# Performance work log

Hardware: AMD Instinct MI355X
Metric: run time of the kernel (lower is better)

Reference implementation:

```python
import jax, jax.numpy as jnp
import numpy as np
from jax import lax

B, S, H, SS, DS = 512, 200, 128, 2, 2  # batch, seq_len, hidden, static_size, dynamic_size

def _xavier(k, shape):
    fan_in, fan_out = shape[-1], shape[0]
    lim = float(np.sqrt(6.0 / (fan_in + fan_out)))
    return jax.random.uniform(k, shape, jnp.float32, -lim, lim)

def setup_inputs() -> dict:
    key = jax.random.key(0)
    ks = jax.random.split(key, 20)
    return {
        "static":  jax.random.uniform(ks[0], (B, SS, S), jnp.float32),
        "dynamic": jax.random.uniform(ks[1], (B, DS, S), jnp.float32),
        # Encoder: 1x1 Conv1d weights stored as [H, C] (kernel dim squeezed)
        "sW": _xavier(ks[2], (H, SS)),  "sb": jnp.zeros((H,), jnp.float32),
        "dW": _xavier(ks[3], (H, DS)),  "db": jnp.zeros((H,), jnp.float32),
        # Decoder learned initial output / hidden
        "x0": _xavier(ks[4], (1, SS)),  "h0": _xavier(ks[5], (1, H)),
        # Decoder input embedding Linear(SS -> H)
        "Wemb": _xavier(ks[6], (H, SS)), "bemb": jnp.zeros((H,), jnp.float32),
        # GRU (1 layer): torch layout [3H, H] gates ordered (r, z, n)
        "Wih": _xavier(ks[7], (3 * H, H)), "Whh": _xavier(ks[8], (3 * H, H)),
        "bih": jnp.zeros((3 * H,), jnp.float32), "bhh": jnp.zeros((3 * H,), jnp.float32),
        # Attention: v [H], W [H, 3H]
        "Wa": _xavier(ks[9], (H, 3 * H)), "va": _xavier(ks[10], (1, H))[0],
        # Decoder pointer head: v [H], W [H, 2H]
        "Wd": _xavier(ks[11], (H, 2 * H)), "vd": _xavier(ks[12], (1, H))[0],
    }

def _decode(static, dynamic, sW, sb, dW, db, x0, h0, Wemb, bemb,
            Wih, Whh, bih, bhh, Wa, va, Wd, vd):
    # Encoder: 1x1 convs == per-node linear maps  -> [B, H, S]
    static_enc  = jnp.einsum('hc,bcs->bhs', sW, static)  + sb[None, :, None]
    dynamic_enc = jnp.einsum('hc,bcs->bhs', dW, dynamic) + db[None, :, None]

    keys = jax.random.split(jax.random.key(42), S)  # one sample key per decode step
    static_sg = lax.stop_gradient(static)           # mirrors static.data gather in torch

    def step(carry, key):
        last_out, h = carry                              # [B,SS], [B,H]
        emb = last_out @ Wemb.T + bemb                   # [B,H]
        # GRU cell (torch gate order r, z, n)
        gi = emb @ Wih.T + bih                           # [B,3H]
        gh = h @ Whh.T + bhh
        r = jax.nn.sigmoid(gi[:, :H] + gh[:, :H])
        z = jax.nn.sigmoid(gi[:, H:2 * H] + gh[:, H:2 * H])
        n = jnp.tanh(gi[:, 2 * H:] + r * gh[:, 2 * H:])
        h_new = (1.0 - z) * n + z * h                    # [B,H]
        # Additive attention over nodes (vectorized over batch)
        hid = jnp.broadcast_to(h_new[:, :, None], (B, H, S))
        energy = jnp.concatenate([static_enc, dynamic_enc, hid], axis=1)   # [B,3H,S]
        attn = jax.nn.softmax(
            jnp.einsum('h,bhs->bs', va, jnp.tanh(jnp.einsum('hk,bks->bhs', Wa, energy))),
            axis=1)                                      # [B,S]
        context = jnp.einsum('bs,bhs->bh', attn, static_enc)               # [B,H]
        ctx = jnp.concatenate(
            [static_enc, jnp.broadcast_to(context[:, :, None], (B, H, S))], axis=1)  # [B,2H,S]
        logits = jnp.einsum('h,bhs->bs', vd,
                            jnp.tanh(jnp.einsum('hk,bks->bhs', Wd, ctx)))  # [B,S]
        # mask is all ones (mask_fn=None) -> log(mask)=0
        probs = jax.nn.softmax(logits, axis=1)
        idx = jax.random.categorical(key, logits, axis=1)                  # [B] int
        next_out = jnp.take_along_axis(static_sg, idx[:, None, None], axis=2)[:, :, 0]  # [B,SS]
        chosen_p = jnp.take_along_axis(probs, idx[:, None], axis=1)[:, 0]  # [B]
        return (next_out, h_new), (idx, chosen_p)

    init = (jnp.broadcast_to(x0, (B, SS)), jnp.broadcast_to(h0, (B, H)))
    _, (idx_seq, prob_seq) = lax.scan(step, init, keys)
    return idx_seq.T, prob_seq.T                          # [B,S] each

def reference(static, dynamic, sW, sb, dW, db, x0, h0, Wemb, bemb,
              Wih, Whh, bih, bhh, Wa, va, Wd, vd):
    return _decode(static, dynamic, sW, sb, dW, db, x0, h0, Wemb, bemb,
                   Wih, Whh, bih, bhh, Wa, va, Wd, vd)
```

## Files before the change

kernel.cpp:

```cpp
#include <hip/hip_runtime.h>
#include <stdint.h>
#include <math.h>

#define NB 512
#define NS 200
#define NH 128
#define NH3 384
#define NWAVE 8

#define IDX4(h) ((h) + (((h) >> 6) << 2))
#define IDX1(h) ((h) + (((h) >> 6) << 4))

__device__ __forceinline__ float xla_tanhf(float x) {
  float cx = fminf(fmaxf(x, -9.0f), 9.0f);
  float x2 = __fmul_rn(cx, cx);
  float p = -2.76076847742355e-16f;
  p = __fadd_rn(__fmul_rn(x2, p), 2.00018790482477e-13f);
  p = __fadd_rn(__fmul_rn(x2, p), -8.60467152213735e-11f);
  p = __fadd_rn(__fmul_rn(x2, p), 5.12229709037114e-08f);
  p = __fadd_rn(__fmul_rn(x2, p), 1.48572235717979e-05f);
  p = __fadd_rn(__fmul_rn(x2, p), 6.37261928875436e-04f);
  p = __fadd_rn(__fmul_rn(x2, p), 4.89352455891786e-03f);
  p = __fmul_rn(cx, p);
  float q = 1.19825839466702e-06f;
  q = __fadd_rn(__fmul_rn(x2, q), 1.18534705686654e-04f);
  q = __fadd_rn(__fmul_rn(x2, q), 2.26843463243900e-03f);
  q = __fadd_rn(__fmul_rn(x2, q), 4.89352518554385e-03f);
  float r = __fdiv_rn(p, q);
  return (fabsf(x) < 0.0004f) ? x : r;
}

__device__ __forceinline__ float xla_sigmoidf(float x) {
  return __fadd_rn(0.5f, __fmul_rn(0.5f, xla_tanhf(__fmul_rn(0.5f, x))));
}

__device__ __forceinline__ float fast_tanhf(float x) {
  float e = __expf(__fmul_rn(x, 2.0f));
  float r = __builtin_amdgcn_rcpf(__fadd_rn(e, 1.0f));
  return fmaf(-2.0f, r, 1.0f);
}

__device__ __forceinline__ uint32_t rotl32(uint32_t v, int r) {
  return (v << r) | (v >> (32 - r));
}
__device__ __forceinline__ void threefry2x32(uint32_t k0, uint32_t k1,
                                             uint32_t x0, uint32_t x1,
                                             uint32_t& o0, uint32_t& o1) {
  uint32_t k2 = k0 ^ k1 ^ 0x1BD11BDAu;
  x0 += k0; x1 += k1;
  #define TFR(r) { x0 += x1; x1 = rotl32(x1, r); x1 ^= x0; }
  TFR(13) TFR(15) TFR(26) TFR(6)
  x0 += k1; x1 += k2 + 1u;
  TFR(17) TFR(29) TFR(16) TFR(24)
  x0 += k2; x1 += k0 + 2u;
  TFR(13) TFR(15) TFR(26) TFR(6)
  x0 += k0; x1 += k1 + 3u;
  TFR(17) TFR(29) TFR(16) TFR(24)
  x0 += k1; x1 += k2 + 4u;
  TFR(13) TFR(15) TFR(26) TFR(6)
  x0 += k2; x1 += k0 + 5u;
  #undef TFR
  o0 = x0; o1 = x1;
}

__device__ __forceinline__ float bits_to_gumbel(uint32_t bits) {
  const float kTiny = 1.1754943508222875e-38f;
  float f = __fsub_rn(__uint_as_float((bits >> 9) | 0x3F800000u), 1.0f);
  float u = __fadd_rn(__fmul_rn(f, __fsub_rn(1.0f, kTiny)), kTiny);
  u = fmaxf(kTiny, u);
  return -logf(-logf(u));
}

__global__ __launch_bounds__(512, 4) void k_decode(
    const float* __restrict__ stat, const float* __restrict__ dyn,
    const float* __restrict__ sW,   const float* __restrict__ sb,
    const float* __restrict__ dW,   const float* __restrict__ db,
    const float* __restrict__ x0,   const float* __restrict__ h0,
    const float* __restrict__ Wemb, const float* __restrict__ bemb,
    const float* __restrict__ Wih,  const float* __restrict__ Whh,
    const float* __restrict__ bih,  const float* __restrict__ bhh,
    const float* __restrict__ Wa,   const float* __restrict__ va,
    const float* __restrict__ Wd,   const float* __restrict__ vd,
    float* __restrict__ out) {

  __shared__ __align__(16) float st0L[NS], st1L[NS], dy0L[NS], dy1L[NS];
  __shared__ float4 AF4p[132];
  __shared__ float4 DF4p[132];
  __shared__ float4 CW4[NH];
  __shared__ float  vaP[144];
  __shared__ float  AcL[NH];
  __shared__ float WembL[2*NH], bembL[NH];
  __shared__ float bihL[NH3], bhhL[NH3];
  __shared__ __align__(16) float embL[NH], hL[NH];
  __shared__ float giL[NH3], ghL[NH3];
  __shared__ float HtLp[144];
  __shared__ float ex2L[NS];
  __shared__ uint32_t keysL[2*NS];
  __shared__ float xpL[2];
  __shared__ float part[NWAVE][8];
  __shared__ int   partI[NWAVE];

  const int t = threadIdx.x;
  const int b = blockIdx.x;
  const int w = t >> 6;
  const int s = t >> 1;
  const int h0i = (t & 1) * 64;
  const int b4 = h0i + ((h0i >> 6) << 2);
  const int b1 = h0i + ((h0i >> 6) << 4);
  const bool activeS = (t < 2*NS);

  if (t < NS) {
    st0L[t] = stat[(size_t)b*2*NS + t];
    st1L[t] = stat[(size_t)b*2*NS + NS + t];
    dy0L[t] = dyn[(size_t)b*2*NS + t];
    dy1L[t] = dyn[(size_t)b*2*NS + NS + t];
    uint32_t q0, q1;
    threefry2x32(0u, 42u, 0u, (uint32_t)t, q0, q1);
    keysL[2*t] = q0; keysL[2*t + 1] = q1;
  }
  if (t < NH) {
    int h = t;
    const float* war = Wa + (size_t)h * NH3;
    float as0 = 0.f, as1 = 0.f, ad0 = 0.f, ad1 = 0.f, ac = 0.f;
    for (int k = 0; k < NH; ++k) {
      as0 = fmaf(war[k],     sW[k*2+0], as0);
      as1 = fmaf(war[k],     sW[k*2+1], as1);
      ad0 = fmaf(war[NH+k],  dW[k*2+0], ad0);
      ad1 = fmaf(war[NH+k],  dW[k*2+1], ad1);
      ac  = fmaf(war[k],     sb[k],     ac);
    }
    for (int k = 0; k < NH; ++k) ac = fmaf(war[NH+k], db[k], ac);
    AF4p[IDX4(h)] = make_float4(as0, as1, ad0, ad1);
    vaP[IDX1(h)] = va[h];
    AcL[h] = ac;

    const float* wdr = Wd + (size_t)h * 256;
    float ds0 = 0.f, ds1 = 0.f, dc = 0.f, c0 = 0.f, c1 = 0.f, cb = 0.f;
    for (int k = 0; k < NH; ++k) {
      ds0 = fmaf(wdr[k],    sW[k*2+0], ds0);
      ds1 = fmaf(wdr[k],    sW[k*2+1], ds1);
      dc  = fmaf(wdr[k],    sb[k],     dc);
      c0  = fmaf(wdr[NH+k], sW[k*2+0], c0);
      c1  = fmaf(wdr[NH+k], sW[k*2+1], c1);
      cb  = fmaf(wdr[NH+k], sb[k],     cb);
    }
    DF4p[IDX4(h)] = make_float4(ds0, ds1, vd[h], dc);
    CW4[h] = make_float4(c0, c1, cb, 0.f);

    bembL[h] = bemb[h];
    WembL[2*h]   = Wemb[2*h];
    WembL[2*h+1] = Wemb[2*h+1];
    hL[h] = h0[h];
  }
  for (int i = t; i < NH3; i += 512) { bihL[i] = bih[i]; bhhL[i] = bhh[i]; }
  if (t == 0) { xpL[0] = x0[0]; xpL[1] = x0[1]; }
  __syncthreads();

  float s0r = 0.f, s1r = 0.f, d0r = 0.f, d1r = 0.f;
  if (activeS) { s0r = st0L[s]; s1r = st1L[s]; d0r = dy0L[s]; d1r = dy1L[s]; }

  for (int step = 0; step < NS; ++step) {
    if (t < NH) {
      float e = fmaf(xpL[1], WembL[t*2+1], __fmul_rn(xpL[0], WembL[t*2+0]));
      embL[t] = __fadd_rn(e, bembL[t]);
    }
    __syncthreads();

    if (t < 256) {
      const float4* wp0 = (const float4*)(Wih + (size_t)t * NH);
      const float4* wp1 = (const float4*)(Whh + (size_t)(NH + t) * NH);
      const float4* e4 = (const float4*)embL;
      const float4* h4 = (const float4*)hL;
      float a0 = 0.f, a1 = 0.f;
      #pragma unroll 8
      for (int k4 = 0; k4 < 32; ++k4) {
        float4 c0 = wp0[k4], c1 = wp1[k4];
        float4 ev = e4[k4],  hv = h4[k4];
        a0 = fmaf(c0.x, ev.x, a0); a0 = fmaf(c0.y, ev.y, a0);
        a0 = fmaf(c0.z, ev.z, a0); a0 = fmaf(c0.w, ev.w, a0);
        a1 = fmaf(c1.x, hv.x, a1); a1 = fmaf(c1.y, hv.y, a1);
        a1 = fmaf(c1.z, hv.z, a1); a1 = fmaf(c1.w, hv.w, a1);
      }
      giL[t]      = __fadd_rn(a0, bihL[t]);
      ghL[NH + t] = __fadd_rn(a1, bhhL[NH + t]);
    } else {
      const bool isWih = (t < NH3);
      const float4* wp = isWih
          ? (const float4*)(Wih + (size_t)t * NH)
          : (const float4*)(Whh + (size_t)(t - NH3) * NH);
      const float4* op = isWih ? (const float4*)embL : (const float4*)hL;
      float a0 = 0.f;
      #pragma unroll 8
      for (int k4 = 0; k4 < 32; ++k4) {
        float4 c = wp[k4], v = op[k4];
        a0 = fmaf(c.x, v.x, a0); a0 = fmaf(c.y, v.y, a0);
        a0 = fmaf(c.z, v.z, a0); a0 = fmaf(c.w, v.w, a0);
      }
      if (isWih) giL[t]       = __fadd_rn(a0, bihL[t]);
      else       ghL[t - NH3] = __fadd_rn(a0, bhhL[t - NH3]);
    }
    __syncthreads();

    if (t < NH) {
      float r = xla_sigmoidf(__fadd_rn(giL[t],      ghL[t]));
      float z = xla_sigmoidf(__fadd_rn(giL[t+NH],   ghL[t+NH]));
      float n = xla_tanhf(__fadd_rn(giL[t+2*NH], __fmul_rn(r, ghL[t+2*NH])));
      float hv = hL[t];
      hL[t] = __fadd_rn(__fmul_rn(__fsub_rn(1.0f, z), n), __fmul_rn(z, hv));
    }
    __syncthreads();

    if (t < NH) {
      const float4* war = (const float4*)(Wa + (size_t)t*NH3 + 2*NH);
      const float4* hn4 = (const float4*)hL;
      float acc = 0.f;
      #pragma unroll 8
      for (int k4 = 0; k4 < 32; ++k4) {
        float4 a = war[k4], hv = hn4[k4];
        acc = fmaf(a.x, hv.x, acc); acc = fmaf(a.y, hv.y, acc);
        acc = fmaf(a.z, hv.z, acc); acc = fmaf(a.w, hv.w, acc);
      }
      HtLp[IDX1(t)] = __fadd_rn(acc, AcL[t]);
    }
    __syncthreads();

    float acc = 0.f;
    if (activeS) {
      #pragma unroll 4
      for (int j = 0; j < 64; ++j) {
        float4 af = AF4p[b4 + j];
        float vah = vaP[b1 + j];
        float ath = HtLp[b1 + j];
        float e = fmaf(af.y, s1r, __fmul_rn(af.x, s0r));
        e = fmaf(af.z, d0r, e);
        e = fmaf(af.w, d1r, e);
        e = __fadd_rn(e, ath);
        acc = fmaf(vah, fast_tanhf(e), acc);
      }
    }
    float sc = activeS ? __fadd_rn(acc, __shfl_xor(acc, 1)) : 0.f;

    float exv = activeS ? __expf(sc) : 0.f;
    {
      float sm = exv;
      float c0 = __fmul_rn(exv, s0r);
      float c1 = __fmul_rn(exv, s1r);
      #pragma unroll
      for (int mm = 2; mm < 64; mm <<= 1) {
        sm = __fadd_rn(sm, __shfl_xor(sm, mm));
        c0 = __fadd_rn(c0, __shfl_xor(c0, mm));
        c1 = __fadd_rn(c1, __shfl_xor(c1, mm));
      }
      if ((t & 63) == 0) { part[w][0] = sm; part[w][1] = c0; part[w][2] = c1; }
    }
    __syncthreads();

    if (t < NH) {
      float sume = part[0][0], r0 = part[0][1], r1 = part[0][2];
      #pragma unroll
      for (int ww = 1; ww < NWAVE; ++ww) {
        sume = __fadd_rn(sume, part[ww][0]);
        r0   = __fadd_rn(r0,   part[ww][1]);
        r1   = __fadd_rn(r1,   part[ww][2]);
      }
      r0 = __fdiv_rn(r0, sume); r1 = __fdiv_rn(r1, sume);
      float4 cw = CW4[t];
      float ct = fmaf(r0, cw.x, fmaf(r1, cw.y, cw.z));
      HtLp[IDX1(t)] = __fadd_rn(DF4p[IDX4(t)].w, ct);
    }
    __syncthreads();

    float accD = 0.f;
    if (activeS) {
      #pragma unroll 4
      for (int j = 0; j < 64; ++j) {
        float4 df = DF4p[b4 + j];
        float ctd = HtLp[b1 + j];
        float d = fmaf(df.y, s1r, __fmul_rn(df.x, s0r));
        d = __fadd_rn(d, ctd);
        accD = fmaf(df.z, fast_tanhf(d), accD);
      }
    }
    float sc2 = activeS ? __fadd_rn(accD, __shfl_xor(accD, 1)) : 0.f;

    float e2 = activeS ? __expf(sc2) : 0.f;
    if (activeS && (t & 1) == 0) ex2L[s] = e2;
    {
      uint32_t k0 = keysL[2*step], k1 = keysL[2*step + 1];
      float gv = -INFINITY;
      int gidx = 1 << 20;
      if (activeS) {
        uint32_t q0, q1;
        threefry2x32(k0, k1, 0u, (uint32_t)(b*NS + s), q0, q1);
        gv = __fadd_rn(bits_to_gumbel(q0 ^ q1), sc2);
        gidx = s;
      }
      float sm = e2;
      #pragma unroll
      for (int mm = 2; mm < 64; mm <<= 1) {
        sm = __fadd_rn(sm, __shfl_xor(sm, mm));
        float ov = __shfl_xor(gv, mm); int oi = __shfl_xor(gidx, mm);
        if (ov > gv || (ov == gv && oi < gidx)) { gv = ov; gidx = oi; }
      }
      if ((t & 63) == 0) { part[w][3] = sm; part[w][4] = gv; partI[w] = gidx; }
    }
    __syncthreads();

    if (t == 0) {
      float bv = part[0][4]; int bi = partI[0];
      float sume2 = part[0][3];
      #pragma unroll
      for (int ww = 1; ww < NWAVE; ++ww) {
        float vv = part[ww][4]; int ii = partI[ww];
        if (vv > bv || (vv == bv && ii < bi)) { bv = vv; bi = ii; }
        sume2 = __fadd_rn(sume2, part[ww][3]);
      }
      out[(size_t)b*NS + step] = (float)bi;
      out[(size_t)NB*NS + (size_t)b*NS + step] = __fdiv_rn(ex2L[bi], sume2);
      xpL[0] = st0L[bi]; xpL[1] = st1L[bi];
    }
    __syncthreads();
  }
}

extern "C" void kernel_launch(void* const* d_in, const int* in_sizes, int n_in,
                              void* d_out, int out_size, void* d_ws, size_t ws_size,
                              hipStream_t stream) {
  (void)in_sizes; (void)n_in; (void)out_size; (void)d_ws; (void)ws_size;
  const float* stat = (const float*)d_in[0];
  const float* dyn  = (const float*)d_in[1];
  const float* sW   = (const float*)d_in[2];
  const float* sb   = (const float*)d_in[3];
  const float* dW   = (const float*)d_in[4];
  const float* db   = (const float*)d_in[5];
  const float* x0   = (const float*)d_in[6];
  const float* h0   = (const float*)d_in[7];
  const float* Wemb = (const float*)d_in[8];
  const float* bemb = (const float*)d_in[9];
  const float* Wih  = (const float*)d_in[10];
  const float* Whh  = (const float*)d_in[11];
  const float* bih  = (const float*)d_in[12];
  const float* bhh  = (const float*)d_in[13];
  const float* Wa   = (const float*)d_in[14];
  const float* va   = (const float*)d_in[15];
  const float* Wd   = (const float*)d_in[16];
  const float* vd   = (const float*)d_in[17];
  float* out = (float*)d_out;

  k_decode<<<NB, 512, 0, stream>>>(stat, dyn, sW, sb, dW, db, x0, h0,
                                   Wemb, bemb, Wih, Whh, bih, bhh,
                                   Wa, va, Wd, vd, out);
}
```

Measured before the change: 6.057 ms.

## Double block to 1024 threads, four lanes per node with interleaved hidden split

Raises the block size from 512 to 1024 threads so that each of the 200 nodes is handled by four lanes instead of two. Each lane covers a quarter of the hidden units, interleaved with stride 4, and the partial scores are combined with two shuffle steps. The GRU matvec now gives one output row per thread across 768 threads, and the padded shared-memory layouts are replaced by packed float2/float4 arrays with the context bias folded into the fma chains. The goal is to shorten the serial per-node tanh loops, at the cost of more waves per block, heavier synchronisation, and possible register pressure under the (1024, 8) launch bounds.

Measured after the change: 6.826 ms. 1.13x slower.

```diff
diff --git a/kernel.cpp b/kernel.cpp
--- a/kernel.cpp
+++ b/kernel.cpp
@@ -6,10 +6,8 @@
 #define NS 200
 #define NH 128
 #define NH3 384
-#define NWAVE 8
-
-#define IDX4(h) ((h) + (((h) >> 6) << 2))
-#define IDX1(h) ((h) + (((h) >> 6) << 4))
+#define NT 1024
+#define NWAVE 16
 
 __device__ __forceinline__ float xla_tanhf(float x) {
   float cx = fminf(fmaxf(x, -9.0f), 9.0f);
@@ -71,7 +69,7 @@
   return -logf(-logf(u));
 }
 
-__global__ __launch_bounds__(512, 4) void k_decode(
+__global__ __launch_bounds__(NT, 8) void k_decode(
     const float* __restrict__ stat, const float* __restrict__ dyn,
     const float* __restrict__ sW,   const float* __restrict__ sb,
     const float* __restrict__ dW,   const float* __restrict__ db,
@@ -84,16 +82,15 @@
     float* __restrict__ out) {
 
   __shared__ __align__(16) float st0L[NS], st1L[NS], dy0L[NS], dy1L[NS];
-  __shared__ float4 AF4p[132];
-  __shared__ float4 DF4p[132];
+  __shared__ float4 AF4[NH];
+  __shared__ float4 DF4[NH];
   __shared__ float4 CW4[NH];
-  __shared__ float  vaP[144];
+  __shared__ float2 HtVa[NH];
   __shared__ float  AcL[NH];
   __shared__ float WembL[2*NH], bembL[NH];
   __shared__ float bihL[NH3], bhhL[NH3];
   __shared__ __align__(16) float embL[NH], hL[NH];
   __shared__ float giL[NH3], ghL[NH3];
-  __shared__ float HtLp[144];
   __shared__ float ex2L[NS];
   __shared__ uint32_t keysL[2*NS];
   __shared__ float xpL[2];
@@ -103,11 +100,9 @@
   const int t = threadIdx.x;
   const int b = blockIdx.x;
   const int w = t >> 6;
-  const int s = t >> 1;
-  const int h0i = (t & 1) * 64;
-  const int b4 = h0i + ((h0i >> 6) << 2);
-  const int b1 = h0i + ((h0i >> 6) << 4);
-  const bool activeS = (t < 2*NS);
+  const int s = t >> 2;
+  const int q = t & 3;
+  const bool activeS = (t < 4*NS);
 
   if (t < NS) {
     st0L[t] = stat[(size_t)b*2*NS + t];
@@ -130,8 +125,8 @@
       ac  = fmaf(war[k],     sb[k],     ac);
     }
     for (int k = 0; k < NH; ++k) ac = fmaf(war[NH+k], db[k], ac);
-    AF4p[IDX4(h)] = make_float4(as0, as1, ad0, ad1);
-    vaP[IDX1(h)] = va[h];
+    AF4[h] = make_float4(as0, as1, ad0, ad1);
+    HtVa[h] = make_float2(va[h], 0.f);
     AcL[h] = ac;
 
     const float* wdr = Wd + (size_t)h * 256;
@@ -144,15 +139,15 @@
       c1  = fmaf(wdr[NH+k], sW[k*2+1], c1);
       cb  = fmaf(wdr[NH+k], sb[k],     cb);
     }
-    DF4p[IDX4(h)] = make_float4(ds0, ds1, vd[h], dc);
-    CW4[h] = make_float4(c0, c1, cb, 0.f);
+    DF4[h] = make_float4(ds0, ds1, vd[h], 0.f);
+    CW4[h] = make_float4(c0, c1, cb, dc);
 
     bembL[h] = bemb[h];
     WembL[2*h]   = Wemb[2*h];
     WembL[2*h+1] = Wemb[2*h+1];
     hL[h] = h0[h];
   }
-  for (int i = t; i < NH3; i += 512) { bihL[i] = bih[i]; bhhL[i] = bhh[i]; }
+  for (int i = t; i < NH3; i += NT) { bihL[i] = bih[i]; bhhL[i] = bhh[i]; }
   if (t == 0) { xpL[0] = x0[0]; xpL[1] = x0[1]; }
   __syncthreads();
 
@@ -166,31 +161,14 @@
     }
     __syncthreads();
 
-    if (t < 256) {
-      const float4* wp0 = (const float4*)(Wih + (size_t)t * NH);
-      const float4* wp1 = (const float4*)(Whh + (size_t)(NH + t) * NH);
-      const float4* e4 = (const float4*)embL;
-      const float4* h4 = (const float4*)hL;
-      float a0 = 0.f, a1 = 0.f;
-      #pragma unroll 8
-      for (int k4 = 0; k4 < 32; ++k4) {
-        float4 c0 = wp0[k4], c1 = wp1[k4];
-        float4 ev = e4[k4],  hv = h4[k4];
-        a0 = fmaf(c0.x, ev.x, a0); a0 = fmaf(c0.y, ev.y, a0);
-        a0 = fmaf(c0.z, ev.z, a0); a0 = fmaf(c0.w, ev.w, a0);
-        a1 = fmaf(c1.x, hv.x, a1); a1 = fmaf(c1.y, hv.y, a1);
-        a1 = fmaf(c1.z, hv.z, a1); a1 = fmaf(c1.w, hv.w, a1);
-      }
-      giL[t]      = __fadd_rn(a0, bihL[t]);
-      ghL[NH + t] = __fadd_rn(a1, bhhL[NH + t]);
-    } else {
+    if (t < 2*NH3) {
       const bool isWih = (t < NH3);
       const float4* wp = isWih
           ? (const float4*)(Wih + (size_t)t * NH)
           : (const float4*)(Whh + (size_t)(t - NH3) * NH);
       const float4* op = isWih ? (const float4*)embL : (const float4*)hL;
       float a0 = 0.f;
-      #pragma unroll 8
+      #pragma unroll 4
       for (int k4 = 0; k4 < 32; ++k4) {
         float4 c = wp[k4], v = op[k4];
         a0 = fmaf(c.x, v.x, a0); a0 = fmaf(c.y, v.y, a0);
@@ -220,25 +198,27 @@
         acc = fmaf(a.x, hv.x, acc); acc = fmaf(a.y, hv.y, acc);
         acc = fmaf(a.z, hv.z, acc); acc = fmaf(a.w, hv.w, acc);
       }
-      HtLp[IDX1(t)] = __fadd_rn(acc, AcL[t]);
+      HtVa[t].y = __fadd_rn(acc, AcL[t]);
     }
     __syncthreads();
 
     float acc = 0.f;
     if (activeS) {
-      #pragma unroll 4
-      for (int j = 0; j < 64; ++j) {
-        float4 af = AF4p[b4 + j];
-        float vah = vaP[b1 + j];
-        float ath = HtLp[b1 + j];
-        float e = fmaf(af.y, s1r, __fmul_rn(af.x, s0r));
+      #pragma unroll 8
+      for (int j = 0; j < 32; ++j) {
+        int h = q + 4*j;
+        float4 af = AF4[h];
+        float2 hv = HtVa[h];
+        float e = fmaf(af.x, s0r, hv.y);
+        e = fmaf(af.y, s1r, e);
         e = fmaf(af.z, d0r, e);
         e = fmaf(af.w, d1r, e);
-        e = __fadd_rn(e, ath);
-        acc = fmaf(vah, fast_tanhf(e), acc);
-      }
-    }
-    float sc = activeS ? __fadd_rn(acc, __shfl_xor(acc, 1)) : 0.f;
+        acc = fmaf(hv.x, fast_tanhf(e), acc);
+      }
+    }
+    float v = __fadd_rn(acc, __shfl_xor(acc, 1));
+    v = __fadd_rn(v, __shfl_xor(v, 2));
+    float sc = activeS ? v : 0.f;
 
     float exv = activeS ? __expf(sc) : 0.f;
     {
@@ -246,7 +226,7 @@
       float c0 = __fmul_rn(exv, s0r);
       float c1 = __fmul_rn(exv, s1r);
       #pragma unroll
-      for (int mm = 2; mm < 64; mm <<= 1) {
+      for (int mm = 4; mm < 64; mm <<= 1) {
         sm = __fadd_rn(sm, __shfl_xor(sm, mm));
         c0 = __fadd_rn(c0, __shfl_xor(c0, mm));
         c1 = __fadd_rn(c1, __shfl_xor(c1, mm));
@@ -266,25 +246,27 @@
       r0 = __fdiv_rn(r0, sume); r1 = __fdiv_rn(r1, sume);
       float4 cw = CW4[t];
       float ct = fmaf(r0, cw.x, fmaf(r1, cw.y, cw.z));
-      HtLp[IDX1(t)] = __fadd_rn(DF4p[IDX4(t)].w, ct);
+      DF4[t].w = __fadd_rn(cw.w, ct);
     }
     __syncthreads();
 
     float accD = 0.f;
     if (activeS) {
-      #pragma unroll 4
-      for (int j = 0; j < 64; ++j) {
-        float4 df = DF4p[b4 + j];
-        float ctd = HtLp[b1 + j];
-        float d = fmaf(df.y, s1r, __fmul_rn(df.x, s0r));
-        d = __fadd_rn(d, ctd);
+      #pragma unroll 8
+      for (int j = 0; j < 32; ++j) {
+        int h = q + 4*j;
+        float4 df = DF4[h];
+        float d = fmaf(df.x, s0r, df.w);
+        d = fmaf(df.y, s1r, d);
         accD = fmaf(df.z, fast_tanhf(d), accD);
       }
     }
-    float sc2 = activeS ? __fadd_rn(accD, __shfl_xor(accD, 1)) : 0.f;
+    float v2 = __fadd_rn(accD, __shfl_xor(accD, 1));
+    v2 = __fadd_rn(v2, __shfl_xor(v2, 2));
+    float sc2 = activeS ? v2 : 0.f;
 
     float e2 = activeS ? __expf(sc2) : 0.f;
-    if (activeS && (t & 1) == 0) ex2L[s] = e2;
+    if (activeS && q == 0) ex2L[s] = e2;
     {
       uint32_t k0 = keysL[2*step], k1 = keysL[2*step + 1];
       float gv = -INFINITY;
@@ -297,7 +279,7 @@
       }
       float sm = e2;
       #pragma unroll
-      for (int mm = 2; mm < 64; mm <<= 1) {
+      for (int mm = 4; mm < 64; mm <<= 1) {
         sm = __fadd_rn(sm, __shfl_xor(sm, mm));
         float ov = __shfl_xor(gv, mm); int oi = __shfl_xor(gidx, mm);
         if (ov > gv || (ov == gv && oi < gidx)) { gv = ov; gidx = oi; }
@@ -347,7 +329,7 @@
   const float* vd   = (const float*)d_in[17];
   float* out = (float*)d_out;
 
-  k_decode<<<NB, 512, 0, stream>>>(stat, dyn, sW, sb, dW, db, x0, h0,
-                                   Wemb, bemb, Wih, Whh, bih, bhh,
-                                   Wa, va, Wd, vd, out);
-}
+  k_decode<<<NB, NT, 0, stream>>>(stat, dyn, sW, sb, dW, db, x0, h0,
+                                  Wemb, bemb, Wih, Whh, bih, bhh,
+                                  Wa, va, Wd, vd, out);
+}
```

## Fold tanh scaling into precomputed weights and precompute Gumbel noise per step

Applied to the files above, without the earlier changes.

Rewrites the attention and pointer score loops using tanh(x)=1-2/(1+e^{2x}). The factor of 2 is folded into the precomputed encoder-projected weights, and the constant sum of v is applied once after the reduction, which removes a multiply and an add per inner iteration. The ht and va values are packed into one float2 array, and the pointer context term is stored in DF4p.w, so each inner iteration does fewer LDS loads. Threefry Gumbel generation moves to otherwise idle threads (t 128..327) during the embedding phase, so it is no longer computed redundantly by both threads of each pair after the scores. The reformulation changes rounding slightly and could affect sampled indices.

Result: faster. 5.892 ms (-2.7%).

```diff
diff --git a/kernel.cpp b/kernel.cpp
--- a/kernel.cpp
+++ b/kernel.cpp
@@ -9,7 +9,7 @@
 #define NWAVE 8
 
 #define IDX4(h) ((h) + (((h) >> 6) << 2))
-#define IDX1(h) ((h) + (((h) >> 6) << 4))
+#define IDX2(h) ((h) + (((h) >> 6) << 3))
 
 __device__ __forceinline__ float xla_tanhf(float x) {
   float cx = fminf(fmaxf(x, -9.0f), 9.0f);
@@ -32,12 +32,6 @@
 
 __device__ __forceinline__ float xla_sigmoidf(float x) {
   return __fadd_rn(0.5f, __fmul_rn(0.5f, xla_tanhf(__fmul_rn(0.5f, x))));
-}
-
-__device__ __forceinline__ float fast_tanhf(float x) {
-  float e = __expf(__fmul_rn(x, 2.0f));
-  float r = __builtin_amdgcn_rcpf(__fadd_rn(e, 1.0f));
-  return fmaf(-2.0f, r, 1.0f);
 }
 
 __device__ __forceinline__ uint32_t rotl32(uint32_t v, int r) {
@@ -87,16 +81,16 @@
   __shared__ float4 AF4p[132];
   __shared__ float4 DF4p[132];
   __shared__ float4 CW4[NH];
-  __shared__ float  vaP[144];
+  __shared__ float2 HtVaP[136];
   __shared__ float  AcL[NH];
   __shared__ float WembL[2*NH], bembL[NH];
   __shared__ float bihL[NH3], bhhL[NH3];
   __shared__ __align__(16) float embL[NH], hL[NH];
   __shared__ float giL[NH3], ghL[NH3];
-  __shared__ float HtLp[144];
-  __shared__ float ex2L[NS];
+  __shared__ float ex2L[NS], gumL[NS];
   __shared__ uint32_t keysL[2*NS];
   __shared__ float xpL[2];
+  __shared__ float SvL[2];
   __shared__ float part[NWAVE][8];
   __shared__ int   partI[NWAVE];
 
@@ -106,7 +100,7 @@
   const int s = t >> 1;
   const int h0i = (t & 1) * 64;
   const int b4 = h0i + ((h0i >> 6) << 2);
-  const int b1 = h0i + ((h0i >> 6) << 4);
+  const int b2 = h0i + ((h0i >> 6) << 3);
   const bool activeS = (t < 2*NS);
 
   if (t < NS) {
@@ -130,8 +124,8 @@
       ac  = fmaf(war[k],     sb[k],     ac);
     }
     for (int k = 0; k < NH; ++k) ac = fmaf(war[NH+k], db[k], ac);
-    AF4p[IDX4(h)] = make_float4(as0, as1, ad0, ad1);
-    vaP[IDX1(h)] = va[h];
+    AF4p[IDX4(h)] = make_float4(2.f*as0, 2.f*as1, 2.f*ad0, 2.f*ad1);
+    HtVaP[IDX2(h)] = make_float2(va[h], 0.f);
     AcL[h] = ac;
 
     const float* wdr = Wd + (size_t)h * 256;
@@ -144,8 +138,8 @@
       c1  = fmaf(wdr[NH+k], sW[k*2+1], c1);
       cb  = fmaf(wdr[NH+k], sb[k],     cb);
     }
-    DF4p[IDX4(h)] = make_float4(ds0, ds1, vd[h], dc);
-    CW4[h] = make_float4(c0, c1, cb, 0.f);
+    DF4p[IDX4(h)] = make_float4(2.f*ds0, 2.f*ds1, vd[h], 0.f);
+    CW4[h] = make_float4(2.f*c0, 2.f*c1, 2.f*cb, 2.f*dc);
 
     bembL[h] = bemb[h];
     WembL[2*h]   = Wemb[2*h];
@@ -153,16 +147,28 @@
     hL[h] = h0[h];
   }
   for (int i = t; i < NH3; i += 512) { bihL[i] = bih[i]; bhhL[i] = bhh[i]; }
-  if (t == 0) { xpL[0] = x0[0]; xpL[1] = x0[1]; }
+  if (t == 0) {
+    xpL[0] = x0[0]; xpL[1] = x0[1];
+    float sva = 0.f, svd = 0.f;
+    for (int h = 0; h < NH; ++h) { sva = __fadd_rn(sva, va[h]); svd = __fadd_rn(svd, vd[h]); }
+    SvL[0] = sva; SvL[1] = svd;
+  }
   __syncthreads();
 
   float s0r = 0.f, s1r = 0.f, d0r = 0.f, d1r = 0.f;
   if (activeS) { s0r = st0L[s]; s1r = st1L[s]; d0r = dy0L[s]; d1r = dy1L[s]; }
+  const float svaR = SvL[0], svdR = SvL[1];
 
   for (int step = 0; step < NS; ++step) {
     if (t < NH) {
       float e = fmaf(xpL[1], WembL[t*2+1], __fmul_rn(xpL[0], WembL[t*2+0]));
       embL[t] = __fadd_rn(e, bembL[t]);
+    } else if (t < NH + NS) {
+      int si = t - NH;
+      uint32_t k0 = keysL[2*step], k1 = keysL[2*step + 1];
+      uint32_t q0, q1;
+      threefry2x32(k0, k1, 0u, (uint32_t)(b*NS + si), q0, q1);
+      gumL[si] = bits_to_gumbel(q0 ^ q1);
     }
     __syncthreads();
 
@@ -220,25 +226,26 @@
         acc = fmaf(a.x, hv.x, acc); acc = fmaf(a.y, hv.y, acc);
         acc = fmaf(a.z, hv.z, acc); acc = fmaf(a.w, hv.w, acc);
       }
-      HtLp[IDX1(t)] = __fadd_rn(acc, AcL[t]);
-    }
-    __syncthreads();
-
-    float acc = 0.f;
+      HtVaP[IDX2(t)].y = __fmul_rn(2.0f, __fadd_rn(acc, AcL[t]));
+    }
+    __syncthreads();
+
+    float accE = 0.f;
     if (activeS) {
       #pragma unroll 4
       for (int j = 0; j < 64; ++j) {
         float4 af = AF4p[b4 + j];
-        float vah = vaP[b1 + j];
-        float ath = HtLp[b1 + j];
-        float e = fmaf(af.y, s1r, __fmul_rn(af.x, s0r));
-        e = fmaf(af.z, d0r, e);
-        e = fmaf(af.w, d1r, e);
-        e = __fadd_rn(e, ath);
-        acc = fmaf(vah, fast_tanhf(e), acc);
-      }
-    }
-    float sc = activeS ? __fadd_rn(acc, __shfl_xor(acc, 1)) : 0.f;
+        float2 hv = HtVaP[b2 + j];
+        float e2 = fmaf(af.x, s0r, hv.y);
+        e2 = fmaf(af.y, s1r, e2);
+        e2 = fmaf(af.z, d0r, e2);
+        e2 = fmaf(af.w, d1r, e2);
+        float r = __builtin_amdgcn_rcpf(__fadd_rn(__expf(e2), 1.0f));
+        accE = fmaf(hv.x, r, accE);
+      }
+    }
+    float accSum = __fadd_rn(accE, __shfl_xor(accE, 1));
+    float sc = activeS ? fmaf(-2.0f, accSum, svaR) : 0.f;
 
     float exv = activeS ? __expf(sc) : 0.f;
     {
@@ -265,8 +272,8 @@
       }
       r0 = __fdiv_rn(r0, sume); r1 = __fdiv_rn(r1, sume);
       float4 cw = CW4[t];
-      float ct = fmaf(r0, cw.x, fmaf(r1, cw.y, cw.z));
-      HtLp[IDX1(t)] = __fadd_rn(DF4p[IDX4(t)].w, ct);
+      float ct2 = fmaf(r0, cw.x, fmaf(r1, cw.y, cw.z));
+      DF4p[IDX4(t)].w = __fadd_rn(cw.w, ct2);
     }
     __syncthreads();
 
@@ -275,24 +282,22 @@
       #pragma unroll 4
       for (int j = 0; j < 64; ++j) {
         float4 df = DF4p[b4 + j];
-        float ctd = HtLp[b1 + j];
-        float d = fmaf(df.y, s1r, __fmul_rn(df.x, s0r));
-        d = __fadd_rn(d, ctd);
-        accD = fmaf(df.z, fast_tanhf(d), accD);
-      }
-    }
-    float sc2 = activeS ? __fadd_rn(accD, __shfl_xor(accD, 1)) : 0.f;
+        float d2 = fmaf(df.x, s0r, df.w);
+        d2 = fmaf(df.y, s1r, d2);
+        float r = __builtin_amdgcn_rcpf(__fadd_rn(__expf(d2), 1.0f));
+        accD = fmaf(df.z, r, accD);
+      }
+    }
+    float accDS = __fadd_rn(accD, __shfl_xor(accD, 1));
+    float sc2 = activeS ? fmaf(-2.0f, accDS, svdR) : 0.f;
 
     float e2 = activeS ? __expf(sc2) : 0.f;
     if (activeS && (t & 1) == 0) ex2L[s] = e2;
     {
-      uint32_t k0 = keysL[2*step], k1 = keysL[2*step + 1];
       float gv = -INFINITY;
       int gidx = 1 << 20;
       if (activeS) {
-        uint32_t q0, q1;
-        threefry2x32(k0, k1, 0u, (uint32_t)(b*NS + s), q0, q1);
-        gv = __fadd_rn(bits_to_gumbel(q0 ^ q1), sc2);
+        gv = __fadd_rn(gumL[s], sc2);
         gidx = s;
       }
       float sm = e2;
```
